# Kernel tuning notes

Measured on AMD Instinct MI355X. Metric: run time of the kernel, lower is better.

Reference implementation:

```python
import jax, jax.numpy as jnp
import numpy as np

K = 7          # kernel_size
PAD = 3        # padding = (K - 1) // 2, stride = 1
H, W = 2048, 2048


def _design_pinv():
    # Same design matrix as the torch module: plane z = C0*x + C1*y + C2
    half = (K - 1) / 2
    space = np.arange(-half, half + 1, 1)
    X, Y = np.meshgrid(space, space)              # 'xy' indexing, matches np.meshgrid default
    A = np.c_[X.flatten(), Y.flatten(), np.ones(K * K)].astype(np.float32)  # [K*K, 3]
    # lstsq with full-column-rank A == pinv(A) @ v
    return jnp.asarray(np.linalg.pinv(A).astype(np.float32))  # [3, K*K]


def setup_inputs() -> dict:
    key = jax.random.key(0)
    x = jax.random.normal(key, (H, W), dtype=jnp.float32)
    return {"x": x}


def reference(x):
    h, w = x.shape
    # ReplicationPad2d == edge padding
    xp = jnp.pad(x, PAD, mode='edge')[None, None]  # [1, 1, h+2P, w+2P]
    # Extract all KxK patches; with 1 input channel the K*K channel dim is
    # kernel-row-major, matching unfold(2,K,1).unfold(3,K,1).view(N, K*K).
    patches = jax.lax.conv_general_dilated_patches(
        xp, (K, K), (1, 1), 'VALID')               # [1, K*K, h, w]
    pv = patches.reshape(K * K, h * w).T            # [h*w, K*K]
    pinvA = _design_pinv()                          # [3, K*K]
    cs = pv @ pinvA.T                               # [h*w, 3] plane coeffs per pixel
    return cs.reshape(h, w, 3)
```

## Files before the change

### kernel.cpp

```cpp
#include <hip/hip_runtime.h>

#define HH 2048
#define WW 2048
#define KK 7
#define PADK 3
#define TILE 32
#define PADT (TILE + 6)
#define IN_STRIDE (PADT + 2)
#define HS_STRIDE (TILE + 1)

__global__ __launch_bounds__(256)
void UnfoldPlainFit_42477226558039_kernel(const float* __restrict__ x,
                                          float* __restrict__ out) {
    __shared__ float sIn[PADT][IN_STRIDE];
    __shared__ float sHs[PADT][HS_STRIDE];
    __shared__ float sHx[PADT][HS_STRIDE];

    const int tileR = blockIdx.y * TILE;
    const int tileC = blockIdx.x * TILE;
    const int tid = threadIdx.x;

    for (int idx = tid; idx < PADT * PADT; idx += 256) {
        int lr = idx / PADT;
        int lc = idx - lr * PADT;
        int gr = tileR - PADK + lr;
        int gc = tileC - PADK + lc;
        gr = max(0, min(HH - 1, gr));
        gc = max(0, min(WW - 1, gc));
        sIn[lr][lc] = x[(size_t)gr * WW + gc];
    }
    __syncthreads();

    for (int idx = tid; idx < PADT * TILE; idx += 256) {
        int lr = idx >> 5;
        int oc = idx & 31;
        float s = 0.f, wx = 0.f;
#pragma unroll
        for (int j = 0; j < KK; ++j) {
            float v = sIn[lr][oc + j];
            s += v;
            wx += (float)(j - PADK) * v;
        }
        sHs[lr][oc] = s;
        sHx[lr][oc] = wx;
    }
    __syncthreads();

    const int oc = tid & 31;
    const int orBase = tid >> 5;
#pragma unroll
    for (int k = 0; k < 4; ++k) {
        int orr = orBase + k * 8;
        float c0 = 0.f, c1 = 0.f, c2 = 0.f;
#pragma unroll
        for (int i = 0; i < KK; ++i) {
            float hs = sHs[orr + i][oc];
            float hx = sHx[orr + i][oc];
            c2 += hs;
            c1 += (float)(i - PADK) * hs;
            c0 += hx;
        }
        c0 *= (1.0f / 196.0f);
        c1 *= (1.0f / 196.0f);
        c2 *= (1.0f / 49.0f);
        int r = tileR + orr;
        int c = tileC + oc;
        float* o = out + ((size_t)r * WW + c) * 3;
        o[0] = c0;
        o[1] = c1;
        o[2] = c2;
    }
}

extern "C" void kernel_launch(void* const* d_in, const int* in_sizes, int n_in,
                              void* d_out, int out_size, void* d_ws, size_t ws_size,
                              hipStream_t stream) {
    const float* x = (const float*)d_in[0];
    float* out = (float*)d_out;
    dim3 grid(WW / TILE, HH / TILE);
    dim3 block(256);
    UnfoldPlainFit_42477226558039_kernel<<<grid, block, 0, stream>>>(x, out);
}
```

Measured before the change: 85.70 us.

## Replace shared-memory tiling with register sliding-window strips and vectorized IO

Drops the LDS tile and the two barriers. Each thread now computes a 4-column by 8-row strip, keeping the horizontal box sums and weighted sums in registers as a rolling 7-row window, updated incrementally along the columns. Input rows are read as float4 and each row's 12 output floats are written as three float4 stores, making the strided 3-channel output writes contiguous. In exchange, each thread rereads 6 halo rows per 8 output rows and uses more registers; the cross-row reuse now relies on cache rather than shared memory.

```diff
diff --git a/kernel.cpp b/kernel.cpp
--- a/kernel.cpp
+++ b/kernel.cpp
@@ -2,73 +2,93 @@
 
 #define HH 2048
 #define WW 2048
-#define KK 7
-#define PADK 3
-#define TILE 32
-#define PADT (TILE + 6)
-#define IN_STRIDE (PADT + 2)
-#define HS_STRIDE (TILE + 1)
+#define RPT 8
+#define CPT 4
+#define NCG (WW / CPT)
+#define NRS (HH / RPT)
 
-__global__ __launch_bounds__(256)
+__global__ __launch_bounds__(256, 2)
 void UnfoldPlainFit_42477226558039_kernel(const float* __restrict__ x,
                                           float* __restrict__ out) {
-    __shared__ float sIn[PADT][IN_STRIDE];
-    __shared__ float sHs[PADT][HS_STRIDE];
-    __shared__ float sHx[PADT][HS_STRIDE];
+    const int g     = blockIdx.x * 256 + threadIdx.x;
+    const int cg    = g & (NCG - 1);
+    const int strip = g >> 9;
+    const int c0    = cg * CPT;
+    const int r0    = strip * RPT;
 
-    const int tileR = blockIdx.y * TILE;
-    const int tileC = blockIdx.x * TILE;
-    const int tid = threadIdx.x;
+    const bool interior = (cg != 0) && (cg != NCG - 1);
 
-    for (int idx = tid; idx < PADT * PADT; idx += 256) {
-        int lr = idx / PADT;
-        int lc = idx - lr * PADT;
-        int gr = tileR - PADK + lr;
-        int gc = tileC - PADK + lc;
+    float s[7][CPT]  = {};
+    float wv[7][CPT] = {};
+
+#pragma unroll
+    for (int i = 0; i < RPT + 6; ++i) {
+        int gr = r0 - 3 + i;
         gr = max(0, min(HH - 1, gr));
-        gc = max(0, min(WW - 1, gc));
-        sIn[lr][lc] = x[(size_t)gr * WW + gc];
-    }
-    __syncthreads();
+        const float* __restrict__ row = x + (size_t)gr * WW;
 
-    for (int idx = tid; idx < PADT * TILE; idx += 256) {
-        int lr = idx >> 5;
-        int oc = idx & 31;
-        float s = 0.f, wx = 0.f;
+        float v[12];
+        if (interior) {
+            const float4 a = *reinterpret_cast<const float4*>(row + c0 - 4);
+            const float4 b = *reinterpret_cast<const float4*>(row + c0);
+            const float4 c = *reinterpret_cast<const float4*>(row + c0 + 4);
+            v[0] = a.x; v[1] = a.y; v[2]  = a.z; v[3]  = a.w;
+            v[4] = b.x; v[5] = b.y; v[6]  = b.z; v[7]  = b.w;
+            v[8] = c.x; v[9] = c.y; v[10] = c.z; v[11] = c.w;
+        } else {
 #pragma unroll
-        for (int j = 0; j < KK; ++j) {
-            float v = sIn[lr][oc + j];
-            s += v;
-            wx += (float)(j - PADK) * v;
+            for (int j = 0; j < 12; ++j) {
+                int gc = c0 - 4 + j;
+                gc = max(0, min(WW - 1, gc));
+                v[j] = row[gc];
+            }
         }
-        sHs[lr][oc] = s;
-        sHx[lr][oc] = wx;
-    }
-    __syncthreads();
 
-    const int oc = tid & 31;
-    const int orBase = tid >> 5;
 #pragma unroll
-    for (int k = 0; k < 4; ++k) {
-        int orr = orBase + k * 8;
-        float c0 = 0.f, c1 = 0.f, c2 = 0.f;
+        for (int k = 0; k < 6; ++k)
 #pragma unroll
-        for (int i = 0; i < KK; ++i) {
-            float hs = sHs[orr + i][oc];
-            float hx = sHx[orr + i][oc];
-            c2 += hs;
-            c1 += (float)(i - PADK) * hs;
-            c0 += hx;
+            for (int cc = 0; cc < CPT; ++cc) {
+                s[k][cc]  = s[k + 1][cc];
+                wv[k][cc] = wv[k + 1][cc];
+            }
+
+        float hs = v[1] + v[2] + v[3] + v[4] + v[5] + v[6] + v[7];
+        float hw = (v[5] - v[3]) + 2.f * (v[6] - v[2]) + 3.f * (v[7] - v[1]);
+        s[6][0]  = hs;
+        wv[6][0] = hw;
+#pragma unroll
+        for (int cc = 1; cc < CPT; ++cc) {
+            const float vl = v[cc];
+            const float vr = v[cc + 7];
+            const float sn = hs - vl + vr;
+            const float wn = hw + 4.f * vl + 3.f * vr - hs;
+            s[6][cc]  = sn;
+            wv[6][cc] = wn;
+            hs = sn;
+            hw = wn;
         }
-        c0 *= (1.0f / 196.0f);
-        c1 *= (1.0f / 196.0f);
-        c2 *= (1.0f / 49.0f);
-        int r = tileR + orr;
-        int c = tileC + oc;
-        float* o = out + ((size_t)r * WW + c) * 3;
-        o[0] = c0;
-        o[1] = c1;
-        o[2] = c2;
+
+        if (i >= 6) {
+            const int r = r0 + (i - 6);
+            float o[12];
+#pragma unroll
+            for (int cc = 0; cc < CPT; ++cc) {
+                const float C2 = s[0][cc] + s[1][cc] + s[2][cc] + s[3][cc]
+                               + s[4][cc] + s[5][cc] + s[6][cc];
+                const float C1 = 3.f * (s[6][cc] - s[0][cc])
+                               + 2.f * (s[5][cc] - s[1][cc])
+                               +       (s[4][cc] - s[2][cc]);
+                const float C0 = wv[0][cc] + wv[1][cc] + wv[2][cc] + wv[3][cc]
+                               + wv[4][cc] + wv[5][cc] + wv[6][cc];
+                o[cc * 3 + 0] = C0 * (1.0f / 196.0f);
+                o[cc * 3 + 1] = C1 * (1.0f / 196.0f);
+                o[cc * 3 + 2] = C2 * (1.0f / 49.0f);
+            }
+            float* __restrict__ op = out + ((size_t)r * WW + c0) * 3;
+            *reinterpret_cast<float4*>(op + 0) = make_float4(o[0], o[1], o[2],  o[3]);
+            *reinterpret_cast<float4*>(op + 4) = make_float4(o[4], o[5], o[6],  o[7]);
+            *reinterpret_cast<float4*>(op + 8) = make_float4(o[8], o[9], o[10], o[11]);
+        }
     }
 }
 
@@ -77,7 +97,8 @@
                               hipStream_t stream) {
     const float* x = (const float*)d_in[0];
     float* out = (float*)d_out;
-    dim3 grid(WW / TILE, HH / TILE);
+    const int total_threads = NCG * NRS;
+    dim3 grid(total_threads / 256);
     dim3 block(256);
     UnfoldPlainFit_42477226558039_kernel<<<grid, block, 0, stream>>>(x, out);
 }
```

After: 85.15 us. No clear change (-0.6%).
